# Kernel optimization log

Measured on AMD Instinct MI355X. Metric: run time of the kernel, lower is better.

## Reference

```python
import jax, jax.numpy as jnp
import numpy as np

B, S, H, N = 2, 2048, 1024, 16
D = H // N


def setup_inputs() -> dict:
    key = jax.random.key(0)
    k1, k2, k3 = jax.random.split(key, 3)
    # Xavier-uniform-ish init for projection weights
    lim_in = (6.0 / (H + 3 * H)) ** 0.5
    lim_out = (6.0 / (H + H)) ** 0.5
    return {
        "hidden_states": jax.random.normal(k1, (B, S, H), dtype=jnp.float32),
        "w_in": jax.random.uniform(k2, (3 * H, H), minval=-lim_in, maxval=lim_in, dtype=jnp.float32),
        "b_in": jnp.zeros((3 * H,), dtype=jnp.float32),
        "w_out": jax.random.uniform(k3, (H, H), minval=-lim_out, maxval=lim_out, dtype=jnp.float32),
        "b_out": jnp.zeros((H,), dtype=jnp.float32),
    }


def reference(hidden_states, w_in, b_in, w_out, b_out):
    b, s, h = hidden_states.shape
    qkv = hidden_states @ w_in.T + b_in  # [B,S,3H]
    q, k, v = jnp.split(qkv, 3, axis=-1)
    # [B,S,H] -> [B,N,S,D]
    def to_heads(x):
        return x.reshape(b, s, N, D).transpose(0, 2, 1, 3)
    q, k, v = to_heads(q), to_heads(k), to_heads(v)
    scale = D ** -0.5
    scores = jnp.einsum("bnqd,bnkd->bnqk", q, k) * scale  # [B,N,S,S]
    causal = jnp.triu(jnp.ones((s, s), dtype=bool), k=1)
    scores = jnp.where(causal, -jnp.inf, scores)
    attn = jax.nn.softmax(scores, axis=-1)
    out = jnp.einsum("bnqk,bnkd->bnqd", attn, v)  # [B,N,S,D]
    out = out.transpose(0, 2, 1, 3).reshape(b, s, h)
    return out @ w_out.T + b_out
```

## Files before the change

kernel.cpp:

```cpp
#include <hip/hip_runtime.h>
#include <hip/hip_bf16.h>

#define BB 2
#define SS 2048
#define HH 1024
#define NH 16
#define DD 64
#define H3 3072
#define MM (BB*SS)

typedef unsigned short u16;
typedef unsigned int u32;
typedef __attribute__((ext_vector_type(8))) short bf16x8;
typedef __attribute__((ext_vector_type(4))) float f32x4;

__device__ __forceinline__ u16 f2bf(float f) {
    union { float f; u32 u; } v; v.f = f;
    u32 u = v.u;
    u += 0x7fffu + ((u >> 16) & 1u);
    return (u16)(u >> 16);
}
__device__ __forceinline__ float bf2f(u16 h) {
    union { u32 u; float f; } v; v.u = ((u32)h) << 16;
    return v.f;
}
__device__ __forceinline__ u32 pack2bf(float a, float b) {
    __hip_bfloat162 h = __float22bfloat162_rn(float2{a, b});
    u32 u; __builtin_memcpy(&u, &h, 4);
    return u;
}
__device__ __forceinline__ void gl_lds16(const void* g, void* l) {
    __builtin_amdgcn_global_load_lds(
        (const __attribute__((address_space(1))) u32*)g,
        (__attribute__((address_space(3))) u32*)l, 16, 0, 0);
}
__device__ __forceinline__ int ginv(int R) {
    return (R & 35) | ((R & 8) << 1) | ((R & 4) << 1) | ((R & 16) >> 2);
}

__global__ void cvt3bf(const float4* __restrict__ s0, uint2* __restrict__ d0, int n0,
                       const float4* __restrict__ s1, uint2* __restrict__ d1, int n1,
                       const float4* __restrict__ s2, uint2* __restrict__ d2, int n2) {
    int i = blockIdx.x * blockDim.x + threadIdx.x;
    const int tot = n0 + n1 + n2;
    for (; i < tot; i += gridDim.x * blockDim.x) {
        const float4* s; uint2* d; int j;
        if (i < n0)            { s = s0; d = d0; j = i; }
        else if (i < n0 + n1)  { s = s1; d = d1; j = i - n0; }
        else                   { s = s2; d = d2; j = i - n0 - n1; }
        float4 v = s[j];
        uint2 o; o.x = pack2bf(v.x, v.y); o.y = pack2bf(v.z, v.w);
        d[j] = o;
    }
}

template<int BN, int MODE>
__global__ __launch_bounds__(256, 3)
void gemm_k2(const u16* __restrict__ A, const u16* __restrict__ Bbf,
             const u16* __restrict__ biasbf, void* __restrict__ Cptr,
             u16* __restrict__ Qo, u16* __restrict__ Ko, u16* __restrict__ Vto,
             int M, int Nn, int K)
{
    constexpr int NFR = BN / 32;
    __shared__ __align__(16) u16 Alds[2][128 * 32];
    __shared__ __align__(16) u16 Blds[2][BN * 32];
    const int tid = threadIdx.x;
    const int w = tid >> 6, lane = tid & 63, quad = lane >> 4, l16 = lane & 15;
    const int m0 = blockIdx.x * 128, n0 = blockIdx.y * BN;
    const int wm = w >> 1, wn = w & 1;
    const int rA4 = lane >> 2, c8b = (lane & 3) * 8;

    f32x4 acc[4][NFR] = {};

#define GSTAGE(k0_, bi_) do {                                                  \
    _Pragma("unroll")                                                          \
    for (int q = 0; q < 2; ++q) {                                              \
        int row0 = w * 32 + q * 16;                                            \
        gl_lds16(&A[(size_t)(m0 + row0 + rA4) * K + (k0_) + c8b],              \
                 &Alds[bi_][row0 * 32]);                                       \
    }                                                                          \
    _Pragma("unroll")                                                          \
    for (int q = 0; q < BN / 64; ++q) {                                        \
        int row0 = w * (BN / 4) + q * 16;                                      \
        gl_lds16(&Bbf[(size_t)(n0 + row0 + rA4) * K + (k0_) + c8b],            \
                 &Blds[bi_][row0 * 32]);                                       \
    }                                                                          \
} while (0)

    const int NT = K >> 5;
    GSTAGE(0, 0);
    for (int t = 0; t < NT; ++t) {
        const int cur = t & 1;
        __syncthreads();
        if (t + 1 < NT) GSTAGE((t + 1) << 5, cur ^ 1);

        bf16x8 af[4], bfr[NFR];
#pragma unroll
        for (int mi = 0; mi < 4; ++mi)
            af[mi] = *(const bf16x8*)&Alds[cur][(wm * 64 + mi * 16 + l16) * 32 + quad * 8];
#pragma unroll
        for (int ni = 0; ni < NFR; ++ni)
            bfr[ni] = *(const bf16x8*)&Blds[cur][(wn * (BN / 2) + ni * 16 + l16) * 32 + quad * 8];
#pragma unroll
        for (int mi = 0; mi < 4; ++mi)
#pragma unroll
            for (int ni = 0; ni < NFR; ++ni)
                acc[mi][ni] = __builtin_amdgcn_mfma_f32_16x16x32_bf16(
                    af[mi], bfr[ni], acc[mi][ni], 0, 0, 0);
    }
#undef GSTAGE

#pragma unroll
    for (int mi = 0; mi < 4; ++mi) {
        int row_b = m0 + wm * 64 + mi * 16 + quad * 4;
#pragma unroll
        for (int ni = 0; ni < NFR; ++ni) {
            int col = n0 + wn * (BN / 2) + ni * 16 + l16;
            float bv = bf2f(biasbf[col]);
            if constexpr (MODE == 1) {
#pragma unroll
                for (int i = 0; i < 4; ++i)
                    ((float*)Cptr)[(size_t)(row_b + i) * Nn + col] = acc[mi][ni][i] + bv;
            } else {
                if (col < 1024) {
#pragma unroll
                    for (int i = 0; i < 4; ++i)
                        Qo[(size_t)(row_b + i) * 1024 + col] =
                            f2bf((acc[mi][ni][i] + bv) * 0.125f);
                } else if (col < 2048) {
#pragma unroll
                    for (int i = 0; i < 4; ++i)
                        Ko[(size_t)(row_b + i) * 1024 + (col - 1024)] =
                            f2bf(acc[mi][ni][i] + bv);
                } else {
                    int d = col - 2048, hh = d >> 6, dd = d & 63;
                    int b = row_b >> 11, s = row_b & 2047;
                    u16 t0 = f2bf(acc[mi][ni][0] + bv), t1 = f2bf(acc[mi][ni][1] + bv);
                    u16 t2 = f2bf(acc[mi][ni][2] + bv), t3 = f2bf(acc[mi][ni][3] + bv);
                    uint2 pk; pk.x = (u32)t0 | ((u32)t1 << 16);
                    pk.y = (u32)t2 | ((u32)t3 << 16);
                    *(uint2*)&Vto[((size_t)((b * 16 + hh) * 64 + dd)) * 2048 + s] = pk;
                }
            }
        }
    }
}

__global__ __launch_bounds__(256, 2)
void attn_v5(const u16* __restrict__ Q, const u16* __restrict__ Kb,
             const u16* __restrict__ Vt, u16* __restrict__ attn_out) {
    const int bid = blockIdx.x;
    const int r8 = bid & 7, qq = bid >> 3;
    const int pr = qq >> 2, g = (qq & 3) * 8 + r8;
    const int h = g & 15, b = g >> 4;
    const int tid = threadIdx.x;
    const int w = tid >> 6, lane = tid & 63, quad = lane >> 4, l16 = lane & 15;
    __shared__ __align__(16) u16 Klds[2][64 * 64];
    __shared__ __align__(16) u16 Vlds[2][64 * 64];

    const int sl = lane >> 3, cch = lane & 7;
    const int rho0 = (2 * w) * 8 + sl, rho1 = (2 * w + 1) * 8 + sl;
    const int gcs = (cch ^ sl) * 8;
    const int kg0 = ginv(rho0), kg1 = ginv(rho1);
    const int ls0 = (2 * w) * 512, ls1 = (2 * w + 1) * 512;
    const int xk0 = (quad ^ (l16 & 7)) * 8;
    const int xk1 = ((quad + 4) ^ (l16 & 7)) * 8;

    for (int half = 0; half < 2; ++half) {
        const int qt = half ? pr : (31 - pr);
        const int q0 = qt * 64;
        const int T = qt + 1;

        const u16* Qb = Q  + (size_t)(b * SS + q0) * 1024 + h * 64;
        const u16* Kg = Kb + (size_t)(b * SS) * 1024 + h * 64;
        const u16* Vg = Vt + (size_t)((b * 16 + h) * 64) * 2048;

#define STAGE_T(kv0_, bi_) do {                                               \
        gl_lds16(&Kg[(size_t)((kv0_) + kg0) * 1024 + gcs], &Klds[bi_][ls0]);  \
        gl_lds16(&Kg[(size_t)((kv0_) + kg1) * 1024 + gcs], &Klds[bi_][ls1]);  \
        gl_lds16(&Vg[(size_t)rho0 * 2048 + (kv0_) + gcs], &Vlds[bi_][ls0]);   \
        gl_lds16(&Vg[(size_t)rho1 * 2048 + (kv0_) + gcs], &Vlds[bi_][ls1]);   \
    } while (0)

        bf16x8 qf0 = *(const bf16x8*)&Qb[(size_t)(w * 16 + l16) * 1024 + quad * 8];
        bf16x8 qf1 = *(const bf16x8*)&Qb[(size_t)(w * 16 + l16) * 1024 + 32 + quad * 8];

        f32x4 oacc[4] = {};
        float lp = 0.f;

        __syncthreads();
        STAGE_T(0, 0);

        for (int t = 0; t < T; ++t) {
            const int cur = t & 1;
            __syncthreads();
            if (t + 1 < T) STAGE_T((t + 1) * 64, cur ^ 1);
            const u16* Kc = Klds[cur];
            const u16* Vc = Vlds[cur];
            f32x4 sacc[4] = {};
#pragma unroll
            for (int ni = 0; ni < 4; ++ni) {
                const int rb = (ni * 16 + l16) * 64;
                bf16x8 kf0 = *(const bf16x8*)&Kc[rb + xk0];
                bf16x8 kf1 = *(const bf16x8*)&Kc[rb + xk1];
                sacc[ni] = __builtin_amdgcn_mfma_f32_16x16x32_bf16(kf0, qf0, sacc[ni], 0, 0, 0);
                sacc[ni] = __builtin_amdgcn_mfma_f32_16x16x32_bf16(kf1, qf1, sacc[ni], 0, 0, 0);
            }
            u32 pk[4][2];
            if (t + 1 < T) {
#pragma unroll
                for (int ni = 0; ni < 4; ++ni) {
                    float p0 = __expf(sacc[ni][0]), p1 = __expf(sacc[ni][1]);
                    float p2 = __expf(sacc[ni][2]), p3 = __expf(sacc[ni][3]);
                    lp += (p0 + p1) + (p2 + p3);
                    pk[ni][0] = pack2bf(p0, p1);
                    pk[ni][1] = pack2bf(p2, p3);
                }
            } else {
                const int thr = w * 16 + l16;
#pragma unroll
                for (int ni = 0; ni < 4; ++ni) {
                    const int pb = 32 * (ni >> 1) + 8 * quad + 4 * (ni & 1);
                    float pv[4];
#pragma unroll
                    for (int i = 0; i < 4; ++i) {
                        float e = __expf(sacc[ni][i]);
                        pv[i] = (pb + i <= thr) ? e : 0.f;
                    }
                    lp += (pv[0] + pv[1]) + (pv[2] + pv[3]);
                    pk[ni][0] = pack2bf(pv[0], pv[1]);
                    pk[ni][1] = pack2bf(pv[2], pv[3]);
                }
            }
            union { u32 u[4]; bf16x8 v; } pf0, pf1;
            pf0.u[0] = pk[0][0]; pf0.u[1] = pk[0][1];
            pf0.u[2] = pk[1][0]; pf0.u[3] = pk[1][1];
            pf1.u[0] = pk[2][0]; pf1.u[1] = pk[2][1];
            pf1.u[2] = pk[3][0]; pf1.u[3] = pk[3][1];
#pragma unroll
            for (int ni = 0; ni < 4; ++ni) {
                const int rb = (ni * 16 + l16) * 64;
                bf16x8 vf0 = *(const bf16x8*)&Vc[rb + xk0];
                bf16x8 vf1 = *(const bf16x8*)&Vc[rb + xk1];
                oacc[ni] = __builtin_amdgcn_mfma_f32_16x16x32_bf16(pf0.v, vf0, oacc[ni], 0, 0, 0);
                oacc[ni] = __builtin_amdgcn_mfma_f32_16x16x32_bf16(pf1.v, vf1, oacc[ni], 0, 0, 0);
            }
        }

        lp += __shfl_xor(lp, 16, 64);
        lp += __shfl_xor(lp, 32, 64);
        float linv[4];
#pragma unroll
        for (int i = 0; i < 4; ++i)
            linv[i] = 1.0f / __shfl(lp, quad * 4 + i, 64);

        u16* ob = attn_out + (size_t)(b * SS + q0 + w * 16) * 1024 + h * 64;
#pragma unroll
        for (int ni = 0; ni < 4; ++ni)
#pragma unroll
            for (int i = 0; i < 4; ++i)
                ob[(size_t)(quad * 4 + i) * 1024 + ni * 16 + l16] =
                    f2bf(oacc[ni][i] * linv[i]);
#undef STAGE_T
    }
}

extern "C" void kernel_launch(void* const* d_in, const int* in_sizes, int n_in,
                              void* d_out, int out_size, void* d_ws, size_t ws_size,
                              hipStream_t stream) {
    const float* hidden = (const float*)d_in[0];
    const float* w_in   = (const float*)d_in[1];
    const float* b_in   = (const float*)d_in[2];
    const float* w_out  = (const float*)d_in[3];
    const float* b_out  = (const float*)d_in[4];
    float* out = (float*)d_out;

    char* ws = (char*)d_ws;
    u16* hid_bf  = (u16*)d_out;
    u16* wi_bf   = (u16*)ws;
    u16* bi_bf   = (u16*)(ws + 6291456);
    u16* attn_ws = (u16*)ws;
    u16* Qbuf    = (u16*)(ws + 8388608);
    u16* wo_bf   = (u16*)(ws + 8388608);
    u16* bo_bf   = (u16*)(ws + 8388608 + 2097152);
    u16* Kbuf    = (u16*)(ws + 16777216);
    u16* Vtbuf   = (u16*)(ws + 25165824);

    cvt3bf<<<dim3(2048), dim3(256), 0, stream>>>(
        (const float4*)hidden, (uint2*)hid_bf, 1048576,
        (const float4*)w_in,   (uint2*)wi_bf,  786432,
        (const float4*)b_in,   (uint2*)bi_bf,  768);
    gemm_k2<128, 2><<<dim3(32, 24), dim3(256), 0, stream>>>(
        hid_bf, wi_bf, bi_bf, nullptr, Qbuf, Kbuf, Vtbuf, MM, H3, HH);
    attn_v5<<<dim3(512), dim3(256), 0, stream>>>(
        Qbuf, Kbuf, Vtbuf, attn_ws);
    cvt3bf<<<dim3(512), dim3(256), 0, stream>>>(
        (const float4*)w_out, (uint2*)wo_bf, 262144,
        (const float4*)b_out, (uint2*)bo_bf, 256,
        nullptr, nullptr, 0);
    gemm_k2<64, 1><<<dim3(32, 16), dim3(256), 0, stream>>>(
        attn_ws, wo_bf, bo_bf, out, nullptr, nullptr, nullptr, MM, HH, HH);
}
```

Measured before the change: 173.9 us.

## Process two 64-row query tiles per block to share K/V tile loads

The attention kernel now handles a 128-row query super-tile per block, with two sets of Q fragments and accumulators reusing each K/V LDS tile. This halves K/V global and LDS traffic per query row. Causal masking is split into diagonal cases via a macro, and the pairing of heavy and light tiles is kept. In exchange the grid drops to 256 blocks with launch bounds of one block per SM, and register pressure roughly doubles, which lowers occupancy and the amount of latency hiding.

```diff
diff --git a/kernel.cpp b/kernel.cpp
--- a/kernel.cpp
+++ b/kernel.cpp
@@ -146,12 +146,12 @@
     }
 }
 
-__global__ __launch_bounds__(256, 2)
-void attn_v5(const u16* __restrict__ Q, const u16* __restrict__ Kb,
+__global__ __launch_bounds__(256, 1)
+void attn_v6(const u16* __restrict__ Q, const u16* __restrict__ Kb,
              const u16* __restrict__ Vt, u16* __restrict__ attn_out) {
     const int bid = blockIdx.x;
     const int r8 = bid & 7, qq = bid >> 3;
-    const int pr = qq >> 2, g = (qq & 3) * 8 + r8;
+    const int pr = qq & 7, g = (qq >> 3) * 8 + r8;
     const int h = g & 15, b = g >> 4;
     const int tid = threadIdx.x;
     const int w = tid >> 6, lane = tid & 63, quad = lane >> 4, l16 = lane & 15;
@@ -165,15 +165,10 @@
     const int ls0 = (2 * w) * 512, ls1 = (2 * w + 1) * 512;
     const int xk0 = (quad ^ (l16 & 7)) * 8;
     const int xk1 = ((quad + 4) ^ (l16 & 7)) * 8;
-
-    for (int half = 0; half < 2; ++half) {
-        const int qt = half ? pr : (31 - pr);
-        const int q0 = qt * 64;
-        const int T = qt + 1;
-
-        const u16* Qb = Q  + (size_t)(b * SS + q0) * 1024 + h * 64;
-        const u16* Kg = Kb + (size_t)(b * SS) * 1024 + h * 64;
-        const u16* Vg = Vt + (size_t)((b * 16 + h) * 64) * 2048;
+    const int thr = w * 16 + l16;
+
+    const u16* Kg = Kb + (size_t)(b * SS) * 1024 + h * 64;
+    const u16* Vg = Vt + (size_t)((b * 16 + h) * 64) * 2048;
 
 #define STAGE_T(kv0_, bi_) do {                                               \
         gl_lds16(&Kg[(size_t)((kv0_) + kg0) * 1024 + gcs], &Klds[bi_][ls0]);  \
@@ -182,87 +177,129 @@
         gl_lds16(&Vg[(size_t)rho1 * 2048 + (kv0_) + gcs], &Vlds[bi_][ls1]);   \
     } while (0)
 
-        bf16x8 qf0 = *(const bf16x8*)&Qb[(size_t)(w * 16 + l16) * 1024 + quad * 8];
-        bf16x8 qf1 = *(const bf16x8*)&Qb[(size_t)(w * 16 + l16) * 1024 + 32 + quad * 8];
-
-        f32x4 oacc[4] = {};
-        float lp = 0.f;
+#define ATTN_TILE(t_, MA_, MB_) do {                                          \
+    const int cur_ = (t_) & 1;                                                \
+    __syncthreads();   \
+    if ((t_) + 1 < T) STAGE_T(((t_) + 1) * 64, cur_ ^ 1);                     \
+    const u16* Kc_ = Klds[cur_];                                              \
+    const u16* Vc_ = Vlds[cur_];                                              \
+    f32x4 sA[4] = {}; f32x4 sB[4] = {};                                       \
+    _Pragma("unroll")                                                         \
+    for (int ni = 0; ni < 4; ++ni) {                                          \
+        const int rb = (ni * 16 + l16) * 64;                                  \
+        bf16x8 kf0 = *(const bf16x8*)&Kc_[rb + xk0];                          \
+        bf16x8 kf1 = *(const bf16x8*)&Kc_[rb + xk1];                          \
+        if ((MA_) != 2) {                                                     \
+            sA[ni] = __builtin_amdgcn_mfma_f32_16x16x32_bf16(kf0, qfA0, sA[ni], 0, 0, 0); \
+            sA[ni] = __builtin_amdgcn_mfma_f32_16x16x32_bf16(kf1, qfA1, sA[ni], 0, 0, 0); \
+        }                                                                     \
+        sB[ni] = __builtin_amdgcn_mfma_f32_16x16x32_bf16(kf0, qfB0, sB[ni], 0, 0, 0); \
+        sB[ni] = __builtin_amdgcn_mfma_f32_16x16x32_bf16(kf1, qfB1, sB[ni], 0, 0, 0); \
+    }                                                                         \
+    u32 pkA[4][2], pkB[4][2];                                                 \
+    _Pragma("unroll")                                                         \
+    for (int ni = 0; ni < 4; ++ni) {                                          \
+        const int pb = 32 * (ni >> 1) + 8 * quad + 4 * (ni & 1);              \
+        if ((MA_) == 0) {                                                     \
+            float p0 = __expf(sA[ni][0]), p1 = __expf(sA[ni][1]);             \
+            float p2 = __expf(sA[ni][2]), p3 = __expf(sA[ni][3]);             \
+            lpA += (p0 + p1) + (p2 + p3);                                     \
+            pkA[ni][0] = pack2bf(p0, p1); pkA[ni][1] = pack2bf(p2, p3);       \
+        } else if ((MA_) == 1) {                                              \
+            float pv[4];                                                      \
+            _Pragma("unroll")                                                 \
+            for (int i = 0; i < 4; ++i) {                                     \
+                float e = __expf(sA[ni][i]);                                  \
+                pv[i] = (pb + i <= thr) ? e : 0.f;                            \
+            }                                                                 \
+            lpA += (pv[0] + pv[1]) + (pv[2] + pv[3]);                         \
+            pkA[ni][0] = pack2bf(pv[0], pv[1]); pkA[ni][1] = pack2bf(pv[2], pv[3]); \
+        }                                                                     \
+        if ((MB_) == 0) {                                                     \
+            float p0 = __expf(sB[ni][0]), p1 = __expf(sB[ni][1]);             \
+            float p2 = __expf(sB[ni][2]), p3 = __expf(sB[ni][3]);             \
+            lpB += (p0 + p1) + (p2 + p3);                                     \
+            pkB[ni][0] = pack2bf(p0, p1); pkB[ni][1] = pack2bf(p2, p3);       \
+        } else {                                                              \
+            float pv[4];                                                      \
+            _Pragma("unroll")                                                 \
+            for (int i = 0; i < 4; ++i) {                                     \
+                float e = __expf(sB[ni][i]);                                  \
+                pv[i] = (pb + i <= thr) ? e : 0.f;                            \
+            }                                                                 \
+            lpB += (pv[0] + pv[1]) + (pv[2] + pv[3]);                         \
+            pkB[ni][0] = pack2bf(pv[0], pv[1]); pkB[ni][1] = pack2bf(pv[2], pv[3]); \
+        }                                                                     \
+    }                                                                         \
+    union { u32 u[4]; bf16x8 v; } pA0, pA1, pB0, pB1;                         \
+    pA0.u[0] = pkA[0][0]; pA0.u[1] = pkA[0][1];                               \
+    pA0.u[2] = pkA[1][0]; pA0.u[3] = pkA[1][1];                               \
+    pA1.u[0] = pkA[2][0]; pA1.u[1] = pkA[2][1];                               \
+    pA1.u[2] = pkA[3][0]; pA1.u[3] = pkA[3][1];                               \
+    pB0.u[0] = pkB[0][0]; pB0.u[1] = pkB[0][1];                               \
+    pB0.u[2] = pkB[1][0]; pB0.u[3] = pkB[1][1];                               \
+    pB1.u[0] = pkB[2][0]; pB1.u[1] = pkB[2][1];                               \
+    pB1.u[2] = pkB[3][0]; pB1.u[3] = pkB[3][1];                               \
+    _Pragma("unroll")                                                         \
+    for (int ni = 0; ni < 4; ++ni) {                                          \
+        const int rb = (ni * 16 + l16) * 64;                                  \
+        bf16x8 vf0 = *(const bf16x8*)&Vc_[rb + xk0];                          \
+        bf16x8 vf1 = *(const bf16x8*)&Vc_[rb + xk1];                          \
+        if ((MA_) != 2) {                                                     \
+            oaccA[ni] = __builtin_amdgcn_mfma_f32_16x16x32_bf16(pA0.v, vf0, oaccA[ni], 0, 0, 0); \
+            oaccA[ni] = __builtin_amdgcn_mfma_f32_16x16x32_bf16(pA1.v, vf1, oaccA[ni], 0, 0, 0); \
+        }                                                                     \
+        oaccB[ni] = __builtin_amdgcn_mfma_f32_16x16x32_bf16(pB0.v, vf0, oaccB[ni], 0, 0, 0); \
+        oaccB[ni] = __builtin_amdgcn_mfma_f32_16x16x32_bf16(pB1.v, vf1, oaccB[ni], 0, 0, 0); \
+    }                                                                         \
+} while (0)
+
+    for (int half = 0; half < 2; ++half) {
+        const int st = half ? pr : (15 - pr);
+        const int Q0 = st * 128;
+        const int u2 = 2 * st;
+        const int T = u2 + 2;
+
+        const u16* Qb = Q + (size_t)(b * SS + Q0) * 1024 + h * 64;
+        bf16x8 qfA0 = *(const bf16x8*)&Qb[(size_t)(w * 16 + l16) * 1024 + quad * 8];
+        bf16x8 qfA1 = *(const bf16x8*)&Qb[(size_t)(w * 16 + l16) * 1024 + 32 + quad * 8];
+        bf16x8 qfB0 = *(const bf16x8*)&Qb[(size_t)(64 + w * 16 + l16) * 1024 + quad * 8];
+        bf16x8 qfB1 = *(const bf16x8*)&Qb[(size_t)(64 + w * 16 + l16) * 1024 + 32 + quad * 8];
+
+        f32x4 oaccA[4] = {}, oaccB[4] = {};
+        float lpA = 0.f, lpB = 0.f;
 
         __syncthreads();
         STAGE_T(0, 0);
 
-        for (int t = 0; t < T; ++t) {
-            const int cur = t & 1;
-            __syncthreads();
-            if (t + 1 < T) STAGE_T((t + 1) * 64, cur ^ 1);
-            const u16* Kc = Klds[cur];
-            const u16* Vc = Vlds[cur];
-            f32x4 sacc[4] = {};
-#pragma unroll
-            for (int ni = 0; ni < 4; ++ni) {
-                const int rb = (ni * 16 + l16) * 64;
-                bf16x8 kf0 = *(const bf16x8*)&Kc[rb + xk0];
-                bf16x8 kf1 = *(const bf16x8*)&Kc[rb + xk1];
-                sacc[ni] = __builtin_amdgcn_mfma_f32_16x16x32_bf16(kf0, qf0, sacc[ni], 0, 0, 0);
-                sacc[ni] = __builtin_amdgcn_mfma_f32_16x16x32_bf16(kf1, qf1, sacc[ni], 0, 0, 0);
+        for (int t = 0; t < u2; ++t) ATTN_TILE(t, 0, 0);
+        ATTN_TILE(u2, 1, 0);
+        ATTN_TILE(u2 + 1, 2, 1);
+
+        lpA += __shfl_xor(lpA, 16, 64);
+        lpA += __shfl_xor(lpA, 32, 64);
+        lpB += __shfl_xor(lpB, 16, 64);
+        lpB += __shfl_xor(lpB, 32, 64);
+        float linvA[4], linvB[4];
+#pragma unroll
+        for (int i = 0; i < 4; ++i) {
+            linvA[i] = 1.0f / __shfl(lpA, quad * 4 + i, 64);
+            linvB[i] = 1.0f / __shfl(lpB, quad * 4 + i, 64);
+        }
+        u16* obA = attn_out + (size_t)(b * SS + Q0 + w * 16) * 1024 + h * 64;
+        u16* obB = obA + (size_t)64 * 1024;
+#pragma unroll
+        for (int ni = 0; ni < 4; ++ni)
+#pragma unroll
+            for (int i = 0; i < 4; ++i) {
+                obA[(size_t)(quad * 4 + i) * 1024 + ni * 16 + l16] =
+                    f2bf(oaccA[ni][i] * linvA[i]);
+                obB[(size_t)(quad * 4 + i) * 1024 + ni * 16 + l16] =
+                    f2bf(oaccB[ni][i] * linvB[i]);
             }
-            u32 pk[4][2];
-            if (t + 1 < T) {
-#pragma unroll
-                for (int ni = 0; ni < 4; ++ni) {
-                    float p0 = __expf(sacc[ni][0]), p1 = __expf(sacc[ni][1]);
-                    float p2 = __expf(sacc[ni][2]), p3 = __expf(sacc[ni][3]);
-                    lp += (p0 + p1) + (p2 + p3);
-                    pk[ni][0] = pack2bf(p0, p1);
-                    pk[ni][1] = pack2bf(p2, p3);
-                }
-            } else {
-                const int thr = w * 16 + l16;
-#pragma unroll
-                for (int ni = 0; ni < 4; ++ni) {
-                    const int pb = 32 * (ni >> 1) + 8 * quad + 4 * (ni & 1);
-                    float pv[4];
-#pragma unroll
-                    for (int i = 0; i < 4; ++i) {
-                        float e = __expf(sacc[ni][i]);
-                        pv[i] = (pb + i <= thr) ? e : 0.f;
-                    }
-                    lp += (pv[0] + pv[1]) + (pv[2] + pv[3]);
-                    pk[ni][0] = pack2bf(pv[0], pv[1]);
-                    pk[ni][1] = pack2bf(pv[2], pv[3]);
-                }
-            }
-            union { u32 u[4]; bf16x8 v; } pf0, pf1;
-            pf0.u[0] = pk[0][0]; pf0.u[1] = pk[0][1];
-            pf0.u[2] = pk[1][0]; pf0.u[3] = pk[1][1];
-            pf1.u[0] = pk[2][0]; pf1.u[1] = pk[2][1];
-            pf1.u[2] = pk[3][0]; pf1.u[3] = pk[3][1];
-#pragma unroll
-            for (int ni = 0; ni < 4; ++ni) {
-                const int rb = (ni * 16 + l16) * 64;
-                bf16x8 vf0 = *(const bf16x8*)&Vc[rb + xk0];
-                bf16x8 vf1 = *(const bf16x8*)&Vc[rb + xk1];
-                oacc[ni] = __builtin_amdgcn_mfma_f32_16x16x32_bf16(pf0.v, vf0, oacc[ni], 0, 0, 0);
-                oacc[ni] = __builtin_amdgcn_mfma_f32_16x16x32_bf16(pf1.v, vf1, oacc[ni], 0, 0, 0);
-            }
-        }
-
-        lp += __shfl_xor(lp, 16, 64);
-        lp += __shfl_xor(lp, 32, 64);
-        float linv[4];
-#pragma unroll
-        for (int i = 0; i < 4; ++i)
-            linv[i] = 1.0f / __shfl(lp, quad * 4 + i, 64);
-
-        u16* ob = attn_out + (size_t)(b * SS + q0 + w * 16) * 1024 + h * 64;
-#pragma unroll
-        for (int ni = 0; ni < 4; ++ni)
-#pragma unroll
-            for (int i = 0; i < 4; ++i)
-                ob[(size_t)(quad * 4 + i) * 1024 + ni * 16 + l16] =
-                    f2bf(oacc[ni][i] * linv[i]);
+    }
+#undef ATTN_TILE
 #undef STAGE_T
-    }
 }
 
 extern "C" void kernel_launch(void* const* d_in, const int* in_sizes, int n_in,
@@ -292,7 +329,7 @@
         (const float4*)b_in,   (uint2*)bi_bf,  768);
     gemm_k2<128, 2><<<dim3(32, 24), dim3(256), 0, stream>>>(
         hid_bf, wi_bf, bi_bf, nullptr, Qbuf, Kbuf, Vtbuf, MM, H3, HH);
-    attn_v5<<<dim3(512), dim3(256), 0, stream>>>(
+    attn_v6<<<dim3(256), dim3(256), 0, stream>>>(
         Qbuf, Kbuf, Vtbuf, attn_ws);
     cvt3bf<<<dim3(512), dim3(256), 0, stream>>>(
         (const float4*)w_out, (uint2*)wo_bf, 262144,
```

Result: slower. 186.0 us (+6.9%).
